# Kernel optimization log

Measured on AMD Instinct MI355X. Metric: run time of the kernel, lower is better.

## Reference

```python
import jax, jax.numpy as jnp
import numpy as np

BIG = 10000000.0

def heaviside(x):
    return (jnp.tanh(BIG * x) + 1.0) * 0.5

def interception(Prec, PET, INSC):
    INSC = jnp.clip(INSC * 5.0, 0.5, 5.0)
    IMAX = jnp.maximum(jnp.minimum(INSC, PET), 0.0)
    INT = jnp.maximum(jnp.minimum(IMAX, Prec), 0.0)
    INR = jnp.maximum(Prec - INT, 0.0)
    return INT, INR

def soil_moisture_store(SMS1, SMSC):
    SMSC = jnp.clip(SMSC * 500.0, 50.0, 500.0)
    return jnp.maximum(jnp.minimum(SMS1, SMSC), 0.0)

def soil_fluxes(PET, INT, INR, COEFF, SQ, SMSC, SUB, CRAK, SMS1):
    COEFF = jnp.clip(COEFF * 400.0, 50.0, 400.0)
    SQ = jnp.clip(SQ * 6.0, 0.0, 6.0)
    SMSC = jnp.clip(SMSC * 500.0, 50.0, 500.0)
    SUB = jnp.clip(SUB, 0.0, 1.0)
    CRAK = jnp.clip(CRAK, 0.0, 1.0)
    cap = COEFF * jnp.exp(-SQ * SMS1 / SMSC)
    RMO = jnp.maximum(heaviside(cap - INR) * INR + heaviside(INR - cap) * cap, 0.0)
    IRUN = jnp.maximum(INR - RMO, 0.0)
    SRUN = jnp.maximum(SUB * (SMS1 / SMSC) * RMO, 0.0)
    REC = jnp.maximum(CRAK * (SMS1 / SMSC) * (RMO - SRUN), 0.0)
    SMF = jnp.maximum(RMO - SRUN - REC, 0.0)
    POT = jnp.maximum(PET - INT, 0.0)
    r = 10.0 * SMS1 / SMSC
    ETS = jnp.maximum(heaviside(r - POT) * POT + heaviside(POT - r) * r, 0.0)
    return RMO, IRUN, SRUN, REC, SMF, ETS

def recharge_calculation(SMS1, SMSC, REC, SMF, ETS):
    SMSC = jnp.clip(SMSC * 500.0, 50.0, 500.0)
    s = SMS1 + SMF - ETS
    RECnew = heaviside(s - SMSC) * (REC + s - SMSC) + heaviside(SMSC - s) * REC
    return jnp.maximum(RECnew, 0.0)

def groundwaterstore(GW1, RecK):
    RecK = jnp.clip(RecK * 0.3, 0.003, 0.3)
    return jnp.maximum(heaviside(GW1) * (RecK * GW1), 0.0)

def _forward(inputs, INSC, COEFF, SQ, SMSC, SUB, CRAK, RecK):
    B, T, _ = inputs.shape
    xs = jnp.transpose(inputs, (1, 0, 2))  # (T, B, 2)

    def step(carry, x):
        SMS1, GW1 = carry  # each (B, 1)
        Prec, PET = x[:, 0:1], x[:, 1:2]
        INT, INR = interception(Prec, PET, INSC)
        SMS1c = soil_moisture_store(SMS1, SMSC)
        RMO, IRUN, SRUN, REC, SMF, ETS = soil_fluxes(PET, INT, INR, COEFF, SQ, SMSC, SUB, CRAK, SMS1c)
        next_SMS = SMS1c + jnp.clip(SMF - ETS, -100000.0, 100000.0)
        RECnew = recharge_calculation(SMS1c, SMSC, REC, SMF, ETS)
        BAS = groundwaterstore(GW1, RecK)
        next_GW = GW1 + jnp.clip(RECnew - BAS, -100000.0, 100000.0)
        return (next_SMS, next_GW), jnp.concatenate([next_SMS, next_GW], axis=1)

    init = (jnp.zeros((B, 1), inputs.dtype), jnp.zeros((B, 1), inputs.dtype))
    _, outs = jax.lax.scan(step, init, xs)  # (T, B, 2)
    outs = jnp.transpose(outs, (1, 0, 2))   # (B, T, 2)
    outs = jnp.roll(outs, shift=1, axis=1)  # state at step t-1 (wrap like tf.roll)
    SMS1 = outs[:, :, 0:1]
    GW1 = outs[:, :, 1:2]
    Prec = inputs[:, :, 0:1]
    PET = inputs[:, :, 1:2]
    INT, INR = interception(Prec, PET, INSC)
    SMS1 = soil_moisture_store(SMS1, SMSC)
    RMO, IRUN, SRUN, REC, SMF, ETS = soil_fluxes(PET, INT, INR, COEFF, SQ, SMSC, SUB, CRAK, SMS1)
    RECnew = recharge_calculation(SMS1, SMSC, REC, SMF, ETS)
    BAS = groundwaterstore(GW1, RecK)
    DR = jnp.maximum(SRUN + IRUN, 0.0)
    GD = jnp.maximum(BAS, 0.0)
    Q = jnp.maximum(DR + GD, 0.0)
    return Q  # (B, T, 1)


def setup_inputs() -> dict:
    key = jax.random.key(0)
    k1, = jax.random.split(key, 1)
    B, T = 4096, 1024
    # Prec in [0, 20) mm/day, PET in [0, 8) mm/day
    u = jax.random.uniform(k1, (B, T, 2), dtype=jnp.float32)
    scale = jnp.array([20.0, 8.0], dtype=jnp.float32)
    inputs = u * scale
    p = lambda v: jnp.full((1,), v, dtype=jnp.float32)
    return {
        "inputs": inputs,
        "INSC": p(0.5), "COEFF": p(0.5), "SQ": p(0.5), "SMSC": p(0.5),
        "SUB": p(0.5), "CRAK": p(0.5), "RecK": p(0.5),
    }


def reference(inputs, INSC, COEFF, SQ, SMSC, SUB, CRAK, RecK):
    return _forward(inputs, INSC, COEFF, SQ, SMSC, SUB, CRAK, RecK)
```

## Files before the change

kernel.cpp:

```cpp
#include <hip/hip_runtime.h>
#include <hip/hip_bf16.h>
#include <math.h>


struct P {
    float INSC, SMSC, RecK, g1, lc, k1, k2, k3, c2;
};

__device__ __forceinline__ P make_params(const float* pINSC, const float* pCOEFF,
                                         const float* pSQ,   const float* pSMSC,
                                         const float* pSUB,  const float* pCRAK,
                                         const float* pRecK) {
    P p;
    p.INSC      = fminf(fmaxf(pINSC[0]  * 5.0f,   0.5f),   5.0f);
    float COEFF = fminf(fmaxf(pCOEFF[0] * 400.0f, 50.0f),  400.0f);
    float SQ    = fminf(fmaxf(pSQ[0]    * 6.0f,   0.0f),   6.0f);
    p.SMSC      = fminf(fmaxf(pSMSC[0]  * 500.0f, 50.0f),  500.0f);
    float SUB   = fminf(fmaxf(pSUB[0],  0.0f), 1.0f);
    float CRAK  = fminf(fmaxf(pCRAK[0], 0.0f), 1.0f);
    p.RecK      = fminf(fmaxf(pRecK[0]  * 0.3f,   0.003f), 0.3f);
    p.g1 = 1.0f - p.RecK;
    p.lc = log2f(COEFF);
    float inv = 1.0f / p.SMSC;
    p.k1 = SUB * inv;
    p.k2 = CRAK * inv;
    p.k3 = 10.0f * inv;
    p.c2 = (-SQ * inv) * 1.44269504088896340736f;
    return p;
}

__device__ __forceinline__ float step(float Prec, float PET, float& sms, float& gw, const P& p) {
    float INT  = fminf(fminf(p.INSC, PET), Prec);
    float INR  = Prec - INT;
    float POT  = PET - INT;
    float S    = fminf(sms, p.SMSC);
    float u    = fmaf(-p.k1, S, 1.0f);
    float v    = fmaf(-p.k2, S, 1.0f);
    float ETS  = fminf(POT, p.k3 * S);
    float SmE  = S - ETS;
    float e    = exp2f(fmaf(p.c2, S, p.lc));
    float RMO  = fminf(INR, e);
    float w    = u * RMO;
    float s2   = fmaf(v, w, SmE);
    float SMF  = v * w;
    float REC  = w - SMF;
    float RECnew = REC + fmaxf(s2 - p.SMSC, 0.0f);
    float BAS  = p.RecK * gw;
    float Q    = (INR - w) + BAS;
    gw  = fmaf(p.g1, gw, RECnew);
    sms = s2;
    return Q;
}

__device__ __forceinline__ void stepw(float Prec, float PET, float& sms, float& gw, const P& p) {
    float INT  = fminf(fminf(p.INSC, PET), Prec);
    float INR  = Prec - INT;
    float POT  = PET - INT;
    float S    = fminf(sms, p.SMSC);
    float u    = fmaf(-p.k1, S, 1.0f);
    float v    = fmaf(-p.k2, S, 1.0f);
    float ETS  = fminf(POT, p.k3 * S);
    float SmE  = S - ETS;
    float e    = exp2f(fmaf(p.c2, S, p.lc));
    float RMO  = fminf(INR, e);
    float w    = u * RMO;
    float s2   = fmaf(v, w, SmE);
    float SMF  = v * w;
    float REC  = w - SMF;
    float RECnew = REC + fmaxf(s2 - p.SMSC, 0.0f);
    gw  = fmaf(p.g1, gw, RECnew);
    sms = s2;
}

__device__ __forceinline__ void dstep(float Prec, float PET,
                                      float& slo, float& shi, float& gw, const P& p) {
    float INT = fminf(fminf(p.INSC, PET), Prec);
    float INR = Prec - INT;
    float POT = PET - INT;
    {
        float S    = fminf(shi, p.SMSC);
        float u    = fmaf(-p.k1, S, 1.0f);
        float v    = fmaf(-p.k2, S, 1.0f);
        float ETS  = fminf(POT, p.k3 * S);
        float SmE  = S - ETS;
        float e    = exp2f(fmaf(p.c2, S, p.lc));
        float RMO  = fminf(INR, e);
        float w    = u * RMO;
        float s2   = fmaf(v, w, SmE);
        float SMF  = v * w;
        float REC  = w - SMF;
        float RECnew = REC + fmaxf(s2 - p.SMSC, 0.0f);
        gw  = fmaf(p.g1, gw, RECnew);
        shi = s2;
    }
    {
        float S    = fminf(slo, p.SMSC);
        float u    = fmaf(-p.k1, S, 1.0f);
        float v    = fmaf(-p.k2, S, 1.0f);
        float ETS  = fminf(POT, p.k3 * S);
        float SmE  = S - ETS;
        float e    = exp2f(fmaf(p.c2, S, p.lc));
        float RMO  = fminf(INR, e);
        float w    = u * RMO;
        slo = fmaf(v, w, SmE);
    }
}

#define MERGE_TOL 0.75f


#define LB(DST, K, NB) do { int _kn = (K) < (NB) ? (K) : (NB) - 1;              \
    _Pragma("unroll") for (int _q = 0; _q < 4; ++_q) DST[_q] = bp[4 * _kn + _q]; } while (0)

#define PIPE4(NB, CB) do { if ((NB) > 0) {                                      \
    LB(B0, 0, (NB)); LB(B1, 1, (NB)); LB(B2, 2, (NB));                          \
    for (int _j = 0; _j < (NB); _j += 4) {                                      \
        LB(B3, _j + 3, (NB)); CB(B0, _j);                                       \
        LB(B0, _j + 4, (NB)); CB(B1, _j + 1);                                   \
        LB(B1, _j + 5, (NB)); CB(B2, _j + 2);                                   \
        LB(B2, _j + 6, (NB)); CB(B3, _j + 3);                                   \
    }                                                                           \
} } while (0)

#define CBW(BUF, J) do { _Pragma("unroll") for (int _m = 0; _m < 4; ++_m) {     \
    stepw(BUF[_m].x, BUF[_m].y, shi, gw, p);                                    \
    stepw(BUF[_m].z, BUF[_m].w, shi, gw, p); } } while (0)

#define CBD(BUF, J) do { _Pragma("unroll") for (int _m = 0; _m < 4; ++_m) {     \
    dstep(BUF[_m].x, BUF[_m].y, slo, shi, gw, p);                               \
    dstep(BUF[_m].z, BUF[_m].w, slo, shi, gw, p); } } while (0)

#define CBM(BUF, J) do { int _tb = 8 * (J);                                     \
    _Pragma("unroll") for (int _m = 0; _m < 4; ++_m) {                          \
    float _qa = step(BUF[_m].x, BUF[_m].y, sms, gw, p);                         \
    float _qb = step(BUF[_m].z, BUF[_m].w, sms, gw, p);                         \
    lds_q[_tb + 2 * _m][l] = _qa; lds_q[_tb + 2 * _m + 1][l] = _qb; } } while (0)

#define CBF(BUF, J) do { _Pragma("unroll") for (int _m = 0; _m < 4; ++_m) {     \
    float _qa = step(BUF[_m].x, BUF[_m].y, sms, gw, p);                         \
    float _qb = step(BUF[_m].z, BUF[_m].w, sms, gw, p);                         \
    orow2[ib0 + 4 * (J) + _m] = make_float2(_qa, _qb); } } while (0)


template<int T, int NC, int W>
__global__ __launch_bounds__(64, 1)
void hir_pass1(const float* __restrict__ inputs,
               const float* __restrict__ pINSC,  const float* __restrict__ pCOEFF,
               const float* __restrict__ pSQ,    const float* __restrict__ pSMSC,
               const float* __restrict__ pSUB,   const float* __restrict__ pCRAK,
               const float* __restrict__ pRecK,
               float* __restrict__ out, float4* __restrict__ st, int B)
{
    __shared__ float lds_q[64][65];
    const int l   = threadIdx.x;
    const int gid = blockIdx.x * 64 + l;
    const int b = gid % B;
    const int c = gid / B;
    if (c >= NC) return;

    P p = make_params(pINSC, pCOEFF, pSQ, pSMSC, pSUB, pCRAK, pRecK);

    const float4* __restrict__ rp = (const float4*)(inputs + (size_t)b * (2 * T));
    float* __restrict__ orow = out + (size_t)b * T;

    constexpr int CH = T / NC;
    const int i1 = (c * CH) >> 1;
    int i0 = i1 - (W >> 1);
    const bool exact = (i0 <= 0);
    if (i0 < 0) i0 = 0;

    float slo = 0.0f, shi = exact ? 0.0f : p.SMSC, gw = 0.0f;
    float4 B0[4], B1[4], B2[4], B3[4];

    {
        const int nb = (i1 - i0) >> 2;
        const float4* bp = rp + i0;
        if (exact) {
            PIPE4(nb, CBW);
            slo = shi;
        } else {
            PIPE4(nb, CBD);
        }
    }
    const bool merged = exact || ((shi - slo) <= MERGE_TOL);
    float sms = exact ? shi : (0.5f * (slo + shi));

    {
        const float4* bp = rp + i1;
        PIPE4(8, CBM);
    }

    st[(size_t)c * B + b] = make_float4(sms, gw, merged ? 1.0f : 0.0f, 0.0f);

    float q0 = 0.0f;
    const bool hasq0 = (c == NC - 1);
    if (hasq0) {
        float4 f0 = rp[0];
        float ss = sms, gg = gw;
        q0 = step(f0.x, f0.y, ss, gg, p);
    }

    __syncthreads();

    const int b0 = b - l;
    const int t1 = c * CH;
    if (c == 0) {
        if (l > 0) {
            for (int j = 0; j < 64; ++j)
                out[(size_t)(b0 + j) * T + l] = lds_q[l][j];
        }
    } else {
        for (int j = 0; j < 64; ++j)
            out[(size_t)(b0 + j) * T + t1 + l] = lds_q[l][j];
    }
    if (hasq0) orow[0] = q0;
}


template<int T, int NC>
__global__ __launch_bounds__(64)
void hir_fixup(const float* __restrict__ inputs,
               const float* __restrict__ pINSC,  const float* __restrict__ pCOEFF,
               const float* __restrict__ pSQ,    const float* __restrict__ pSMSC,
               const float* __restrict__ pSUB,   const float* __restrict__ pCRAK,
               const float* __restrict__ pRecK,
               float* __restrict__ out, const float4* __restrict__ st, int B)
{
    const int gid = blockIdx.x * 64 + threadIdx.x;
    const int b = gid % B;
    const int c = gid / B;
    if (c >= NC) return;

    float4 sc = st[(size_t)c * B + b];
    if (sc.z != 0.0f) return;

    P p = make_params(pINSC, pCOEFF, pSQ, pSMSC, pSUB, pCRAK, pRecK);
    constexpr int CH = T / NC;

    const float4* __restrict__ rp = (const float4*)(inputs + (size_t)b * (2 * T));
    float* __restrict__ orow = out + (size_t)b * T;
    float2* __restrict__ orow2 = (float2*)orow;

    int m = c - 1;
    float4 sm = st[(size_t)m * B + b];
    while (sm.z == 0.0f) { --m; sm = st[(size_t)m * B + b]; }
    float sms = sm.x, gw = sm.y;

    float4 B0[4], B1[4], B2[4], B3[4];

    {
        const int ia = ((m + 1) * CH) >> 1;
        const int ibx = (c * CH) >> 1;
        const int nb = (ibx - ia) >> 2;
        const float4* bp = rp + ia;
        float& shi = sms;
        PIPE4(nb, CBW);
    }

    {
        const int ib0 = (c * CH) >> 1;
        const float4* bp = rp + ib0;
        PIPE4(8, CBF);
    }

    if (c == NC - 1) {
        float4 f0 = rp[0];
        float ss = sms, gg = gw;
        orow[0] = step(f0.x, f0.y, ss, gg, p);
    }
}

template<int T>
__global__ __launch_bounds__(64, 1)
void hir_scan_kernel(const float* __restrict__ inputs,
                     const float* __restrict__ pINSC,  const float* __restrict__ pCOEFF,
                     const float* __restrict__ pSQ,    const float* __restrict__ pSMSC,
                     const float* __restrict__ pSUB,   const float* __restrict__ pCRAK,
                     const float* __restrict__ pRecK,
                     float* __restrict__ out, int B)
{
    int b = blockIdx.x * blockDim.x + threadIdx.x;
    if (b >= B) return;
    P p = make_params(pINSC, pCOEFF, pSQ, pSMSC, pSUB, pCRAK, pRecK);
    const float4* __restrict__ rp = (const float4*)(inputs + (size_t)b * (2 * T));
    float* __restrict__ orow = out + (size_t)b * T;
    float sms = 0.0f, gw = 0.0f;
    float4 cur = rp[0];
    const float P0 = cur.x, E0 = cur.y;
    constexpr int NI = T / 2;
    for (int i = 0; i < NI; ++i) {
        int ni = (i + 1 < NI) ? (i + 1) : i;
        float4 nxt = rp[ni];
        float qa = step(cur.x, cur.y, sms, gw, p);
        float qb = step(cur.z, cur.w, sms, gw, p);
        if (i == 0) { orow[1] = qb; }
        else        { ((float2*)orow)[i] = make_float2(qa, qb); }
        cur = nxt;
    }
    float ss = sms, gg = gw;
    orow[0] = step(P0, E0, ss, gg, p);
}

extern "C" void kernel_launch(void* const* d_in, const int* in_sizes, int n_in,
                              void* d_out, int out_size, void* d_ws, size_t ws_size,
                              hipStream_t stream) {
    (void)n_in; (void)out_size;
    constexpr int T  = 1024;
    constexpr int NC = 16;
    constexpr int W  = 320;
    const float* inputs = (const float*)d_in[0];
    const float* INSC   = (const float*)d_in[1];
    const float* COEFF  = (const float*)d_in[2];
    const float* SQ     = (const float*)d_in[3];
    const float* SMSC   = (const float*)d_in[4];
    const float* SUB    = (const float*)d_in[5];
    const float* CRAK   = (const float*)d_in[6];
    const float* RecK   = (const float*)d_in[7];
    float* out = (float*)d_out;

    int B = in_sizes[0] / (2 * T);
    size_t stBytes = (size_t)B * NC * sizeof(float4);

    if ((B % 64) == 0 && ws_size >= stBytes) {
        float4* st = (float4*)d_ws;
        long total = (long)B * NC;
        int blocks = (int)((total + 63) / 64);
        hir_pass1<T, NC, W><<<dim3(blocks), dim3(64), 0, stream>>>(
            inputs, INSC, COEFF, SQ, SMSC, SUB, CRAK, RecK, out, st, B);
        hir_fixup<T, NC><<<dim3(blocks), dim3(64), 0, stream>>>(
            inputs, INSC, COEFF, SQ, SMSC, SUB, CRAK, RecK, out, st, B);
        return;
    }

    int blocks = (B + 63) / 64;
    hir_scan_kernel<T><<<dim3(blocks), dim3(64), 0, stream>>>(
        inputs, INSC, COEFF, SQ, SMSC, SUB, CRAK, RecK, out, B);
}
```

Measured before the change: 129.6 us.

## Interleave two independent batch rows per thread in pass1 for ILP

Pass1 now has each thread process two batch rows (b and b+H) with their recurrences interleaved, which gives two independent dependency chains for instruction-level parallelism on the serial scan. It halves the number of pass1 threads and doubles LDS staging. Both kernels also move from a 4-deep to a 3-deep load pipeline to reduce register pressure. The cost is fewer waves in flight and higher register use, which could hurt latency hiding given the launch_bounds(64,1) setting.

After: 141.3 us. 9.0% more time.

```diff
diff --git a/kernel.cpp b/kernel.cpp
--- a/kernel.cpp
+++ b/kernel.cpp
@@ -109,37 +109,67 @@
 #define MERGE_TOL 0.75f
 
 
-#define LB(DST, K, NB) do { int _kn = (K) < (NB) ? (K) : (NB) - 1;              \
+#define LBS(DST, K, NB) do { int _kn = (K) < (NB) ? (K) : (NB) - 1;             \
     _Pragma("unroll") for (int _q = 0; _q < 4; ++_q) DST[_q] = bp[4 * _kn + _q]; } while (0)
 
-#define PIPE4(NB, CB) do { if ((NB) > 0) {                                      \
-    LB(B0, 0, (NB)); LB(B1, 1, (NB)); LB(B2, 2, (NB));                          \
-    for (int _j = 0; _j < (NB); _j += 4) {                                      \
-        LB(B3, _j + 3, (NB)); CB(B0, _j);                                       \
-        LB(B0, _j + 4, (NB)); CB(B1, _j + 1);                                   \
-        LB(B1, _j + 5, (NB)); CB(B2, _j + 2);                                   \
-        LB(B2, _j + 6, (NB)); CB(B3, _j + 3);                                   \
+#define PIPE3S(NB, CB) do { if ((NB) > 0) {                                     \
+    LBS(B0, 0, (NB)); LBS(B1, 1, (NB));                                         \
+    int _j = 0;                                                                 \
+    for (; _j + 3 <= (NB); _j += 3) {                                           \
+        LBS(B2, _j + 2, (NB)); CB(B0, _j);                                      \
+        LBS(B0, _j + 3, (NB)); CB(B1, _j + 1);                                  \
+        LBS(B1, _j + 4, (NB)); CB(B2, _j + 2);                                  \
     }                                                                           \
+    if (_j < (NB)) { LBS(B2, _j + 2, (NB)); CB(B0, _j); ++_j;                   \
+        if (_j < (NB)) { LBS(B0, _j + 2, (NB)); CB(B1, _j); } }                 \
 } } while (0)
 
-#define CBW(BUF, J) do { _Pragma("unroll") for (int _m = 0; _m < 4; ++_m) {     \
+#define CBW1(BUF, J) do { _Pragma("unroll") for (int _m = 0; _m < 4; ++_m) {    \
     stepw(BUF[_m].x, BUF[_m].y, shi, gw, p);                                    \
     stepw(BUF[_m].z, BUF[_m].w, shi, gw, p); } } while (0)
 
-#define CBD(BUF, J) do { _Pragma("unroll") for (int _m = 0; _m < 4; ++_m) {     \
-    dstep(BUF[_m].x, BUF[_m].y, slo, shi, gw, p);                               \
-    dstep(BUF[_m].z, BUF[_m].w, slo, shi, gw, p); } } while (0)
-
-#define CBM(BUF, J) do { int _tb = 8 * (J);                                     \
-    _Pragma("unroll") for (int _m = 0; _m < 4; ++_m) {                          \
-    float _qa = step(BUF[_m].x, BUF[_m].y, sms, gw, p);                         \
-    float _qb = step(BUF[_m].z, BUF[_m].w, sms, gw, p);                         \
-    lds_q[_tb + 2 * _m][l] = _qa; lds_q[_tb + 2 * _m + 1][l] = _qb; } } while (0)
-
-#define CBF(BUF, J) do { _Pragma("unroll") for (int _m = 0; _m < 4; ++_m) {     \
+#define CBF1(BUF, J) do { _Pragma("unroll") for (int _m = 0; _m < 4; ++_m) {    \
     float _qa = step(BUF[_m].x, BUF[_m].y, sms, gw, p);                         \
     float _qb = step(BUF[_m].z, BUF[_m].w, sms, gw, p);                         \
     orow2[ib0 + 4 * (J) + _m] = make_float2(_qa, _qb); } } while (0)
+
+
+#define LBD(DA, DZ, K, NB) do { int _kn = (K) < (NB) ? (K) : (NB) - 1;          \
+    _Pragma("unroll") for (int _q = 0; _q < 4; ++_q) {                          \
+        DA[_q] = bpA[4 * _kn + _q]; DZ[_q] = bpB[4 * _kn + _q]; } } while (0)
+
+#define PIPE3D(NB, CB) do { if ((NB) > 0) {                                     \
+    LBD(A0, Z0, 0, (NB)); LBD(A1, Z1, 1, (NB));                                 \
+    int _j = 0;                                                                 \
+    for (; _j + 3 <= (NB); _j += 3) {                                           \
+        LBD(A2, Z2, _j + 2, (NB)); CB(A0, Z0, _j);                              \
+        LBD(A0, Z0, _j + 3, (NB)); CB(A1, Z1, _j + 1);                          \
+        LBD(A1, Z1, _j + 4, (NB)); CB(A2, Z2, _j + 2);                          \
+    }                                                                           \
+    if (_j < (NB)) { LBD(A2, Z2, _j + 2, (NB)); CB(A0, Z0, _j); ++_j;           \
+        if (_j < (NB)) { LBD(A0, Z0, _j + 2, (NB)); CB(A1, Z1, _j); } }         \
+} } while (0)
+
+#define CBW2(BA, BZ, J) do { _Pragma("unroll") for (int _m = 0; _m < 4; ++_m) { \
+    stepw(BA[_m].x, BA[_m].y, shiA, gwA, p);                                    \
+    stepw(BZ[_m].x, BZ[_m].y, shiB, gwB, p);                                    \
+    stepw(BA[_m].z, BA[_m].w, shiA, gwA, p);                                    \
+    stepw(BZ[_m].z, BZ[_m].w, shiB, gwB, p); } } while (0)
+
+#define CBD2(BA, BZ, J) do { _Pragma("unroll") for (int _m = 0; _m < 4; ++_m) { \
+    dstep(BA[_m].x, BA[_m].y, sloA, shiA, gwA, p);                              \
+    dstep(BZ[_m].x, BZ[_m].y, sloB, shiB, gwB, p);                              \
+    dstep(BA[_m].z, BA[_m].w, sloA, shiA, gwA, p);                              \
+    dstep(BZ[_m].z, BZ[_m].w, sloB, shiB, gwB, p); } } while (0)
+
+#define CBM2(BA, BZ, J) do { int _tb = 8 * (J);                                 \
+    _Pragma("unroll") for (int _m = 0; _m < 4; ++_m) {                          \
+    float _qa = step(BA[_m].x, BA[_m].y, smsA, gwA, p);                         \
+    float _qc = step(BZ[_m].x, BZ[_m].y, smsB, gwB, p);                         \
+    float _qb = step(BA[_m].z, BA[_m].w, smsA, gwA, p);                         \
+    float _qd = step(BZ[_m].z, BZ[_m].w, smsB, gwB, p);                         \
+    lds_qA[_tb + 2 * _m][l] = _qa; lds_qA[_tb + 2 * _m + 1][l] = _qb;           \
+    lds_qB[_tb + 2 * _m][l] = _qc; lds_qB[_tb + 2 * _m + 1][l] = _qd; } } while (0)
 
 
 template<int T, int NC, int W>
@@ -151,17 +181,21 @@
                const float* __restrict__ pRecK,
                float* __restrict__ out, float4* __restrict__ st, int B)
 {
-    __shared__ float lds_q[64][65];
+    __shared__ float lds_qA[64][65];
+    __shared__ float lds_qB[64][65];
     const int l   = threadIdx.x;
     const int gid = blockIdx.x * 64 + l;
-    const int b = gid % B;
-    const int c = gid / B;
+    const int H = B >> 1;
+    const int b = gid % H;
+    const int c = gid / H;
     if (c >= NC) return;
 
     P p = make_params(pINSC, pCOEFF, pSQ, pSMSC, pSUB, pCRAK, pRecK);
 
-    const float4* __restrict__ rp = (const float4*)(inputs + (size_t)b * (2 * T));
-    float* __restrict__ orow = out + (size_t)b * T;
+    const float4* __restrict__ rpA = (const float4*)(inputs + (size_t)b * (2 * T));
+    const float4* __restrict__ rpB = (const float4*)(inputs + (size_t)(b + H) * (2 * T));
+    float* __restrict__ orowA = out + (size_t)b * T;
+    float* __restrict__ orowB = out + (size_t)(b + H) * T;
 
     constexpr int CH = T / NC;
     const int i1 = (c * CH) >> 1;
@@ -169,35 +203,44 @@
     const bool exact = (i0 <= 0);
     if (i0 < 0) i0 = 0;
 
-    float slo = 0.0f, shi = exact ? 0.0f : p.SMSC, gw = 0.0f;
-    float4 B0[4], B1[4], B2[4], B3[4];
+    float sloA = 0.0f, shiA = exact ? 0.0f : p.SMSC, gwA = 0.0f;
+    float sloB = 0.0f, shiB = exact ? 0.0f : p.SMSC, gwB = 0.0f;
+    float4 A0[4], A1[4], A2[4], Z0[4], Z1[4], Z2[4];
 
     {
         const int nb = (i1 - i0) >> 2;
-        const float4* bp = rp + i0;
+        const float4* bpA = rpA + i0;
+        const float4* bpB = rpB + i0;
         if (exact) {
-            PIPE4(nb, CBW);
-            slo = shi;
+            PIPE3D(nb, CBW2);
+            sloA = shiA; sloB = shiB;
         } else {
-            PIPE4(nb, CBD);
+            PIPE3D(nb, CBD2);
         }
     }
-    const bool merged = exact || ((shi - slo) <= MERGE_TOL);
-    float sms = exact ? shi : (0.5f * (slo + shi));
-
-    {
-        const float4* bp = rp + i1;
-        PIPE4(8, CBM);
-    }
-
-    st[(size_t)c * B + b] = make_float4(sms, gw, merged ? 1.0f : 0.0f, 0.0f);
-
-    float q0 = 0.0f;
+    const bool mergedA = exact || ((shiA - sloA) <= MERGE_TOL);
+    const bool mergedB = exact || ((shiB - sloB) <= MERGE_TOL);
+    float smsA = exact ? shiA : (0.5f * (sloA + shiA));
+    float smsB = exact ? shiB : (0.5f * (sloB + shiB));
+
+    {
+        const float4* bpA = rpA + i1;
+        const float4* bpB = rpB + i1;
+        PIPE3D(8, CBM2);
+    }
+
+    st[(size_t)c * B + b]     = make_float4(smsA, gwA, mergedA ? 1.0f : 0.0f, 0.0f);
+    st[(size_t)c * B + b + H] = make_float4(smsB, gwB, mergedB ? 1.0f : 0.0f, 0.0f);
+
+    float q0A = 0.0f, q0B = 0.0f;
     const bool hasq0 = (c == NC - 1);
     if (hasq0) {
-        float4 f0 = rp[0];
-        float ss = sms, gg = gw;
-        q0 = step(f0.x, f0.y, ss, gg, p);
+        float4 f0 = rpA[0];
+        float ss = smsA, gg = gwA;
+        q0A = step(f0.x, f0.y, ss, gg, p);
+        float4 g0 = rpB[0];
+        float tt = smsB, hh = gwB;
+        q0B = step(g0.x, g0.y, tt, hh, p);
     }
 
     __syncthreads();
@@ -206,14 +249,18 @@
     const int t1 = c * CH;
     if (c == 0) {
         if (l > 0) {
-            for (int j = 0; j < 64; ++j)
-                out[(size_t)(b0 + j) * T + l] = lds_q[l][j];
+            for (int j = 0; j < 64; ++j) {
+                out[(size_t)(b0 + j) * T + l]     = lds_qA[l][j];
+                out[(size_t)(b0 + H + j) * T + l] = lds_qB[l][j];
+            }
         }
     } else {
-        for (int j = 0; j < 64; ++j)
-            out[(size_t)(b0 + j) * T + t1 + l] = lds_q[l][j];
-    }
-    if (hasq0) orow[0] = q0;
+        for (int j = 0; j < 64; ++j) {
+            out[(size_t)(b0 + j) * T + t1 + l]     = lds_qA[l][j];
+            out[(size_t)(b0 + H + j) * T + t1 + l] = lds_qB[l][j];
+        }
+    }
+    if (hasq0) { orowA[0] = q0A; orowB[0] = q0B; }
 }
 
 
@@ -246,7 +293,7 @@
     while (sm.z == 0.0f) { --m; sm = st[(size_t)m * B + b]; }
     float sms = sm.x, gw = sm.y;
 
-    float4 B0[4], B1[4], B2[4], B3[4];
+    float4 B0[4], B1[4], B2[4];
 
     {
         const int ia = ((m + 1) * CH) >> 1;
@@ -254,13 +301,13 @@
         const int nb = (ibx - ia) >> 2;
         const float4* bp = rp + ia;
         float& shi = sms;
-        PIPE4(nb, CBW);
+        PIPE3S(nb, CBW1);
     }
 
     {
         const int ib0 = (c * CH) >> 1;
         const float4* bp = rp + ib0;
-        PIPE4(8, CBF);
+        PIPE3S(8, CBF1);
     }
 
     if (c == NC - 1) {
@@ -321,13 +368,15 @@
     int B = in_sizes[0] / (2 * T);
     size_t stBytes = (size_t)B * NC * sizeof(float4);
 
-    if ((B % 64) == 0 && ws_size >= stBytes) {
+    if ((B % 128) == 0 && ws_size >= stBytes) {
         float4* st = (float4*)d_ws;
-        long total = (long)B * NC;
-        int blocks = (int)((total + 63) / 64);
-        hir_pass1<T, NC, W><<<dim3(blocks), dim3(64), 0, stream>>>(
+        long totalP = (long)(B / 2) * NC;
+        int blocksP = (int)((totalP + 63) / 64);
+        hir_pass1<T, NC, W><<<dim3(blocksP), dim3(64), 0, stream>>>(
             inputs, INSC, COEFF, SQ, SMSC, SUB, CRAK, RecK, out, st, B);
-        hir_fixup<T, NC><<<dim3(blocks), dim3(64), 0, stream>>>(
+        long totalF = (long)B * NC;
+        int blocksF = (int)((totalF + 63) / 64);
+        hir_fixup<T, NC><<<dim3(blocksF), dim3(64), 0, stream>>>(
             inputs, INSC, COEFF, SQ, SMSC, SUB, CRAK, RecK, out, st, B);
         return;
     }
```
